# Performance work log

Measured on AMD Instinct MI355X. Metric: run time of the kernel, lower is better.

The kernel has to match this reference:

```python
import jax, jax.numpy as jnp
import numpy as np
import math

IN_SIZE = 4096
OUT_SIZE = 4096
NNZ = 4_194_304
BATCH = 4096


def setup_inputs() -> dict:
    key = jax.random.key(0)
    k_x, k_v, k_i, k_o = jax.random.split(key, 4)
    x = jax.random.normal(k_x, (BATCH, IN_SIZE), dtype=jnp.float32)
    # v = randn(nnz) * (6 / sqrt(in_size + out_size))  (init=None branch)
    scale = 6.0 / math.sqrt(IN_SIZE + OUT_SIZE)
    values = jax.random.normal(k_v, (NNZ,), dtype=jnp.float32) * scale
    idx_in = jax.random.randint(k_i, (NNZ,), 0, IN_SIZE, dtype=jnp.int64 if jax.config.jax_enable_x64 else jnp.int32)
    idx_out = jax.random.randint(k_o, (NNZ,), 0, OUT_SIZE, dtype=jnp.int64 if jax.config.jax_enable_x64 else jnp.int32)
    return {"x": x, "values": values, "idx_in": idx_in, "idx_out": idx_out}


def reference(x, values, idx_in, idx_out):
    # torch.sparse.mm(W, x.T).T with W = coo((idx_out, idx_in), values, (out, in)).
    # Duplicate (row,col) entries in COO sum, which x.at[...].add reproduces.
    # Scattering into a dense [out, in] matrix (64 MB) is the efficient JAX form;
    # it avoids any [nnz, batch] intermediate and then uses one dense GEMM.
    W = jnp.zeros((OUT_SIZE, IN_SIZE), dtype=values.dtype).at[idx_out, idx_in].add(values)
    return x @ W.T  # [batch, out_size]
```

## Files before the change

kernel.cpp:

```cpp
#include <hip/hip_runtime.h>
#include <hip/hip_bf16.h>

#define IN_SIZE 4096
#define OUT_SIZE 4096
#define BATCH 4096

#define NBLK 512
#define CHUNK 8192
#define NCELL 1024
#define CELLCAP 8192

typedef __bf16 bf16x8 __attribute__((ext_vector_type(8)));
typedef float f32x4 __attribute__((ext_vector_type(4)));

__global__ __launch_bounds__(256) void zero_kernel(int* __restrict__ cellcnt) {
    cellcnt[blockIdx.x * 256 + threadIdx.x & 1023] = 0;
}

__global__ __launch_bounds__(512) void scatres_kernel(const float* __restrict__ vals,
                                                      const int* __restrict__ iin,
                                                      const int* __restrict__ iout,
                                                      int* __restrict__ cellcnt,
                                                      uint2* __restrict__ bkt, int nnz) {
    __shared__ int sout[CHUNK];
    __shared__ int hist[NCELL];
    __shared__ int gbase[NCELL];
    const int b = blockIdx.x, tid = threadIdx.x;
    const int base = b * CHUNK;

    for (int c = tid; c < NCELL; c += 512) hist[c] = 0;
    __syncthreads();

    const int4* io4 = (const int4*)(iout + base);
    for (int i = tid; i < CHUNK / 4; i += 512) {
        if (base + i * 4 + 3 < nnz) {
            const int4 o = io4[i];
            ((int4*)sout)[i] = o;
            atomicAdd(&hist[o.x >> 2], 1);
            atomicAdd(&hist[o.y >> 2], 1);
            atomicAdd(&hist[o.z >> 2], 1);
            atomicAdd(&hist[o.w >> 2], 1);
        } else {
            for (int j = 0; j < 4; ++j) {
                const int k = base + i * 4 + j;
                if (k < nnz) {
                    const int o = iout[k];
                    sout[i * 4 + j] = o;
                    atomicAdd(&hist[o >> 2], 1);
                }
            }
        }
    }
    __syncthreads();

    for (int c = tid; c < NCELL; c += 512)
        gbase[c] = hist[c] ? atomicAdd(&cellcnt[c], hist[c]) : 0;
    __syncthreads();

    const float4* v4 = (const float4*)(vals + base);
    const int4*   a4 = (const int4*)(iin + base);
    for (int i = tid; i < CHUNK / 4; i += 512) {
        if (base + i * 4 + 3 < nnz) {
            const float4 v = v4[i];
            const int4   a = a4[i];
            const int4   o = ((const int4*)sout)[i];
            int c, l; uint2 e;
            c = o.x >> 2; l = atomicSub(&hist[c], 1) - 1;
            e.x = __builtin_bit_cast(unsigned, v.x); e.y = (unsigned)(((o.x & 3) << 12) | a.x);
            bkt[(size_t)c * CELLCAP + gbase[c] + l] = e;
            c = o.y >> 2; l = atomicSub(&hist[c], 1) - 1;
            e.x = __builtin_bit_cast(unsigned, v.y); e.y = (unsigned)(((o.y & 3) << 12) | a.y);
            bkt[(size_t)c * CELLCAP + gbase[c] + l] = e;
            c = o.z >> 2; l = atomicSub(&hist[c], 1) - 1;
            e.x = __builtin_bit_cast(unsigned, v.z); e.y = (unsigned)(((o.z & 3) << 12) | a.z);
            bkt[(size_t)c * CELLCAP + gbase[c] + l] = e;
            c = o.w >> 2; l = atomicSub(&hist[c], 1) - 1;
            e.x = __builtin_bit_cast(unsigned, v.w); e.y = (unsigned)(((o.w & 3) << 12) | a.w);
            bkt[(size_t)c * CELLCAP + gbase[c] + l] = e;
        } else {
            for (int j = 0; j < 4; ++j) {
                const int k = base + i * 4 + j;
                if (k < nnz) {
                    const int o = sout[i * 4 + j];
                    const int c = o >> 2;
                    const int l = atomicSub(&hist[c], 1) - 1;
                    uint2 e;
                    e.x = __builtin_bit_cast(unsigned, vals[k]);
                    e.y = (unsigned)(((o & 3) << 12) | iin[k]);
                    bkt[(size_t)c * CELLCAP + gbase[c] + l] = e;
                }
            }
        }
    }
}

__global__ __launch_bounds__(512) void accum_kernel(const uint2* __restrict__ bkt,
                                                    const int* __restrict__ cellcnt,
                                                    __bf16* __restrict__ W,
                                                    const f32x4* __restrict__ xin,
                                                    bf16x8* __restrict__ xout) {
    __shared__ float acc[4 * 4096];
    const int cell = blockIdx.x, tid = threadIdx.x;
    for (int t = tid; t < 4 * 4096; t += 512) acc[t] = 0.f;
    int n = cellcnt[cell];
    if (n > CELLCAP) n = CELLCAP;
    __syncthreads();

    const uint2* seg = bkt + (size_t)cell * CELLCAP;
    for (int s = tid; s < n; s += 512) {
        const uint2 e = seg[s];
        atomicAdd(&acc[((e.y >> 12) & 3u) * 4096 + (e.y & 0xFFFu)],
                  __builtin_bit_cast(float, e.x));
    }
    __syncthreads();

    bf16x8* out = (bf16x8*)(W + (size_t)cell * 4 * 4096);
    for (int t = tid; t < 2048; t += 512) {
        bf16x8 o;
#pragma unroll
        for (int j = 0; j < 8; ++j) o[j] = (__bf16)acc[t * 8 + j];
        out[t] = o;
    }

    const int xbase = blockIdx.x * 2048;
    for (int t = tid; t < 2048; t += 512) {
        const int idx = xbase + t;
        const f32x4 a = xin[2 * idx];
        const f32x4 bq = xin[2 * idx + 1];
        bf16x8 o;
        o[0] = (__bf16)a[0];  o[1] = (__bf16)a[1];  o[2] = (__bf16)a[2];  o[3] = (__bf16)a[3];
        o[4] = (__bf16)bq[0]; o[5] = (__bf16)bq[1]; o[6] = (__bf16)bq[2]; o[7] = (__bf16)bq[3];
        xout[idx] = o;
    }
}


#define GLL(SRC, DST)                                                         \
    __builtin_amdgcn_global_load_lds(                                         \
        (const __attribute__((address_space(1))) void*)(SRC),                 \
        (__attribute__((address_space(3))) void*)(DST), 16, 0, 0)

#define STAGE_AB(T, BUF)                                                      \
  do {                                                                        \
    const __bf16* sa_ = gA0 + (size_t)(T) * 32;                               \
    __bf16* da_ = &smem[(BUF) * 16384 + tid * 8];                             \
    GLL(sa_, da_);                                                            \
    GLL(sa_ + (size_t)524288, da_ + 4096);                                    \
    const __bf16* sb_ = gB0 + (size_t)(T) * 32;                               \
    __bf16* db_ = &smem[(BUF) * 16384 + 8192 + tid * 8];                      \
    GLL(sb_, db_);                                                            \
    GLL(sb_ + (size_t)524288, db_ + 4096);                                    \
  } while (0)

#define VMW4  asm volatile("s_waitcnt vmcnt(4)" ::: "memory")
#define VMW0  asm volatile("s_waitcnt vmcnt(0)" ::: "memory")
#define VMWN  ((void)0)

#define LBFR(D, BUF)                                                          \
    _Pragma("unroll") for (int j_ = 0; j_ < 4; ++j_)                          \
        D[j_] = *(const bf16x8*)(smem + (BUF) * 16384 + offB[j_])
#define LA03(D, BUF)                                                          \
    _Pragma("unroll") for (int i_ = 0; i_ < 4; ++i_)                          \
        D[i_] = *(const bf16x8*)(smem + (BUF) * 16384 + offA[i_])
#define LA47(BUF)                                                             \
    _Pragma("unroll") for (int i_ = 0; i_ < 4; ++i_)                          \
        af47[i_] = *(const bf16x8*)(smem + (BUF) * 16384 + offA[4 + i_])

#define MFMA_C1(CA, CB)                                                       \
    _Pragma("unroll") for (int i_ = 0; i_ < 4; ++i_)                          \
        _Pragma("unroll") for (int j_ = 0; j_ < 4; ++j_)                      \
            acc[i_][j_] = __builtin_amdgcn_mfma_f32_16x16x32_bf16(            \
                CA[i_], CB[j_], acc[i_][j_], 0, 0, 0)
#define MFMA_C2(CB)                                                           \
    _Pragma("unroll") for (int i_ = 0; i_ < 4; ++i_)                          \
        _Pragma("unroll") for (int j_ = 0; j_ < 4; ++j_)                      \
            acc[4 + i_][j_] = __builtin_amdgcn_mfma_f32_16x16x32_bf16(        \
                af47[i_], CB[j_], acc[4 + i_][j_], 0, 0, 0)

#define ITER(T, BUFC, BUFN, CB, CA, NB, NA, DOSTAGE, SBUF, VMW, DOBAR)        \
  do {                                                                        \
    if (DOSTAGE) STAGE_AB((T) + 3, SBUF);                                     \
    LA47(BUFC);                                                               \
    MFMA_C1(CA, CB);                                                          \
    LBFR(NB, BUFN);                                                           \
    LA03(NA, BUFN);                                                           \
    MFMA_C2(CB);                                                              \
    VMW;                                                                      \
    if (DOBAR) __builtin_amdgcn_s_barrier();                                  \
  } while (0)

__global__ __launch_bounds__(512, 2) void gemm_bt_kernel(
    const __bf16* __restrict__ A,
    const __bf16* __restrict__ B,
    float* __restrict__ C) {
    __shared__ __bf16 smem[4 * 16384];

    const int tid   = threadIdx.x;
    const int lane  = tid & 63;
    const int wv    = tid >> 6;
    const int wm    = wv >> 2;
    const int wn    = wv & 3;
    const int row16 = lane & 15;
    const int quad  = lane >> 4;

    const int swz = (blockIdx.x & 7) * 32 + (blockIdx.x >> 3);
    const int bm  = (swz >> 4) * 256;
    const int bn  = (swz & 15) * 256;

    const int sr = tid >> 2;
    const int sq = (tid & 3) ^ ((sr >> 1) & 3);
    const __bf16* gA0 = A + (size_t)(bm + sr) * 4096 + sq * 8;
    const __bf16* gB0 = B + (size_t)(bn + sr) * 4096 + sq * 8;

    int offA[8], offB[4];
#pragma unroll
    for (int i = 0; i < 8; ++i) {
        const int ra = wm * 128 + i * 16 + row16;
        offA[i] = ra * 32 + ((quad ^ ((ra >> 1) & 3)) * 8);
    }
#pragma unroll
    for (int j = 0; j < 4; ++j) {
        const int rb = wn * 64 + j * 16 + row16;
        offB[j] = 8192 + rb * 32 + ((quad ^ ((rb >> 1) & 3)) * 8);
    }

    f32x4  acc[8][4] = {};
    bf16x8 bfr0[4], a0_[4], bfr1[4], a1_[4], af47[4];

    STAGE_AB(0, 0); STAGE_AB(1, 1); STAGE_AB(2, 2);
    VMW4;
    __builtin_amdgcn_s_barrier();
    LBFR(bfr0, 0);
    LA03(a0_, 0);

    for (int c = 0; c < 31; ++c) {
        const int tb = c * 4;
        ITER(tb + 0, 0, 1, bfr0, a0_, bfr1, a1_, 1, 3, VMW4, 1);
        ITER(tb + 1, 1, 2, bfr1, a1_, bfr0, a0_, 1, 0, VMW4, 1);
        ITER(tb + 2, 2, 3, bfr0, a0_, bfr1, a1_, 1, 1, VMW4, 1);
        ITER(tb + 3, 3, 0, bfr1, a1_, bfr0, a0_, 1, 2, VMW4, 1);
    }
    ITER(124, 0, 1, bfr0, a0_, bfr1, a1_, 1, 3, VMW4, 1);
    ITER(125, 1, 2, bfr1, a1_, bfr0, a0_, 0, 0, VMW0, 1);
    ITER(126, 2, 3, bfr0, a0_, bfr1, a1_, 0, 0, VMWN, 0);
    LA47(3);
    MFMA_C1(a1_, bfr1);
    MFMA_C2(bfr1);

#pragma unroll
    for (int i = 0; i < 8; ++i) {
        const int rbase = bm + wm * 128 + i * 16 + quad * 4;
#pragma unroll
        for (int j = 0; j < 4; ++j) {
            const int col = bn + wn * 64 + j * 16 + row16;
#pragma unroll
            for (int r = 0; r < 4; ++r)
                C[(size_t)(rbase + r) * 4096 + col] = acc[i][j][r];
        }
    }
}

extern "C" void kernel_launch(void* const* d_in, const int* in_sizes, int n_in,
                              void* d_out, int out_size, void* d_ws, size_t ws_size,
                              hipStream_t stream) {
    const float* x    = (const float*)d_in[0];
    const float* vals = (const float*)d_in[1];
    const int*   iin  = (const int*)d_in[2];
    const int*   iout = (const int*)d_in[3];
    float*       C    = (float*)d_out;
    const int    nnz  = in_sizes[1];

    char*   ws      = (char*)d_ws;
    __bf16* Wb      = (__bf16*)ws;
    __bf16* Xb      = (__bf16*)(ws + ((size_t)32 << 20));
    int*    cellcnt = (int*)(ws + ((size_t)64 << 20));
    uint2*  bkt     = (uint2*)d_out;

    zero_kernel<<<4, 256, 0, stream>>>(cellcnt);
    scatres_kernel<<<NBLK, 512, 0, stream>>>(vals, iin, iout, cellcnt, bkt, nnz);
    accum_kernel<<<NCELL, 512, 0, stream>>>(bkt, cellcnt, Wb, (const f32x4*)x, (bf16x8*)Xb);
    gemm_bt_kernel<<<256, 512, 0, stream>>>(Xb, Wb, C);
}
```

Measured before the change: 337.2 us.

## Restructure GEMM main loop into barrier-separated phases with MFMA priority boosts

Replaces the register double-buffered fragment pipeline with a phased schedule: each K-step loads A0-3 and B fragments, issues half the global-to-LDS staging, barriers, then runs MFMAs at raised wave priority, and repeats for A4-7 and the other staging half. Splitting the A and B staging across phases and using s_setprio is meant to keep the waves in lockstep and interleave memory with MFMA work across the two resident blocks. This drops the cross-iteration register prefetch and adds several barriers per step, which could expose LDS read latency.

```diff
diff --git a/kernel.cpp b/kernel.cpp
--- a/kernel.cpp
+++ b/kernel.cpp
@@ -140,12 +140,16 @@
         (const __attribute__((address_space(1))) void*)(SRC),                 \
         (__attribute__((address_space(3))) void*)(DST), 16, 0, 0)
 
-#define STAGE_AB(T, BUF)                                                      \
+#define STAGE_A2(T, BUF)                                                      \
   do {                                                                        \
     const __bf16* sa_ = gA0 + (size_t)(T) * 32;                               \
     __bf16* da_ = &smem[(BUF) * 16384 + tid * 8];                             \
     GLL(sa_, da_);                                                            \
     GLL(sa_ + (size_t)524288, da_ + 4096);                                    \
+  } while (0)
+
+#define STAGE_B2(T, BUF)                                                      \
+  do {                                                                        \
     const __bf16* sb_ = gB0 + (size_t)(T) * 32;                               \
     __bf16* db_ = &smem[(BUF) * 16384 + 8192 + tid * 8];                      \
     GLL(sb_, db_);                                                            \
@@ -155,38 +159,47 @@
 #define VMW4  asm volatile("s_waitcnt vmcnt(4)" ::: "memory")
 #define VMW0  asm volatile("s_waitcnt vmcnt(0)" ::: "memory")
 #define VMWN  ((void)0)
-
-#define LBFR(D, BUF)                                                          \
+#define PH_BAR __builtin_amdgcn_s_barrier()
+
+#define LBFR(BUF)                                                             \
     _Pragma("unroll") for (int j_ = 0; j_ < 4; ++j_)                          \
-        D[j_] = *(const bf16x8*)(smem + (BUF) * 16384 + offB[j_])
-#define LA03(D, BUF)                                                          \
-    _Pragma("unroll") for (int i_ = 0; i_ < 4; ++i_)                          \
-        D[i_] = *(const bf16x8*)(smem + (BUF) * 16384 + offA[i_])
+        bfr[j_] = *(const bf16x8*)(smem + (BUF) * 16384 + offB[j_])
+#define LA03(BUF)                                                             \
+    _Pragma("unroll") for (int i_ = 0; i_ < 4; ++i_)                          \
+        af03[i_] = *(const bf16x8*)(smem + (BUF) * 16384 + offA[i_])
 #define LA47(BUF)                                                             \
     _Pragma("unroll") for (int i_ = 0; i_ < 4; ++i_)                          \
         af47[i_] = *(const bf16x8*)(smem + (BUF) * 16384 + offA[4 + i_])
 
-#define MFMA_C1(CA, CB)                                                       \
+#define MFMA_C1                                                               \
     _Pragma("unroll") for (int i_ = 0; i_ < 4; ++i_)                          \
         _Pragma("unroll") for (int j_ = 0; j_ < 4; ++j_)                      \
             acc[i_][j_] = __builtin_amdgcn_mfma_f32_16x16x32_bf16(            \
-                CA[i_], CB[j_], acc[i_][j_], 0, 0, 0)
-#define MFMA_C2(CB)                                                           \
+                af03[i_], bfr[j_], acc[i_][j_], 0, 0, 0)
+#define MFMA_C2                                                               \
     _Pragma("unroll") for (int i_ = 0; i_ < 4; ++i_)                          \
         _Pragma("unroll") for (int j_ = 0; j_ < 4; ++j_)                      \
             acc[4 + i_][j_] = __builtin_amdgcn_mfma_f32_16x16x32_bf16(        \
-                af47[i_], CB[j_], acc[4 + i_][j_], 0, 0, 0)
-
-#define ITER(T, BUFC, BUFN, CB, CA, NB, NA, DOSTAGE, SBUF, VMW, DOBAR)        \
+                af47[i_], bfr[j_], acc[4 + i_][j_], 0, 0, 0)
+
+#define ITER(T, BUF, SBUF, DOSTAGE, VMW, ENDBAR)                              \
   do {                                                                        \
-    if (DOSTAGE) STAGE_AB((T) + 3, SBUF);                                     \
-    LA47(BUFC);                                                               \
-    MFMA_C1(CA, CB);                                                          \
-    LBFR(NB, BUFN);                                                           \
-    LA03(NA, BUFN);                                                           \
-    MFMA_C2(CB);                                                              \
+    LBFR(BUF);                                                                \
+    LA03(BUF);                                                                \
+    if (DOSTAGE) STAGE_A2((T) + 3, SBUF);                                     \
+    PH_BAR;                                                                   \
+    __builtin_amdgcn_s_setprio(1);                                            \
+    MFMA_C1;                                                                  \
+    __builtin_amdgcn_s_setprio(0);                                            \
+    PH_BAR;                                                                   \
+    LA47(BUF);                                                                \
+    if (DOSTAGE) STAGE_B2((T) + 3, SBUF);                                     \
+    PH_BAR;                                                                   \
+    __builtin_amdgcn_s_setprio(1);                                            \
+    MFMA_C2;                                                                  \
+    __builtin_amdgcn_s_setprio(0);                                            \
     VMW;                                                                      \
-    if (DOBAR) __builtin_amdgcn_s_barrier();                                  \
+    if (ENDBAR) PH_BAR;                                                       \
   } while (0)
 
 __global__ __launch_bounds__(512, 2) void gemm_bt_kernel(
@@ -225,27 +238,25 @@
     }
 
     f32x4  acc[8][4] = {};
-    bf16x8 bfr0[4], a0_[4], bfr1[4], a1_[4], af47[4];
-
-    STAGE_AB(0, 0); STAGE_AB(1, 1); STAGE_AB(2, 2);
+    bf16x8 bfr[4], af03[4], af47[4];
+
+    STAGE_A2(0, 0); STAGE_B2(0, 0);
+    STAGE_A2(1, 1); STAGE_B2(1, 1);
+    STAGE_A2(2, 2); STAGE_B2(2, 2);
     VMW4;
-    __builtin_amdgcn_s_barrier();
-    LBFR(bfr0, 0);
-    LA03(a0_, 0);
+    PH_BAR;
 
     for (int c = 0; c < 31; ++c) {
         const int tb = c * 4;
-        ITER(tb + 0, 0, 1, bfr0, a0_, bfr1, a1_, 1, 3, VMW4, 1);
-        ITER(tb + 1, 1, 2, bfr1, a1_, bfr0, a0_, 1, 0, VMW4, 1);
-        ITER(tb + 2, 2, 3, bfr0, a0_, bfr1, a1_, 1, 1, VMW4, 1);
-        ITER(tb + 3, 3, 0, bfr1, a1_, bfr0, a0_, 1, 2, VMW4, 1);
-    }
-    ITER(124, 0, 1, bfr0, a0_, bfr1, a1_, 1, 3, VMW4, 1);
-    ITER(125, 1, 2, bfr1, a1_, bfr0, a0_, 0, 0, VMW0, 1);
-    ITER(126, 2, 3, bfr0, a0_, bfr1, a1_, 0, 0, VMWN, 0);
-    LA47(3);
-    MFMA_C1(a1_, bfr1);
-    MFMA_C2(bfr1);
+        ITER(tb + 0, 0, 3, 1, VMW4, 1);
+        ITER(tb + 1, 1, 0, 1, VMW4, 1);
+        ITER(tb + 2, 2, 1, 1, VMW4, 1);
+        ITER(tb + 3, 3, 2, 1, VMW4, 1);
+    }
+    ITER(124, 0, 3, 1, VMW4, 1);
+    ITER(125, 1, 0, 0, VMW4, 1);
+    ITER(126, 2, 0, 0, VMW0, 1);
+    ITER(127, 3, 0, 0, VMWN, 0);
 
 #pragma unroll
     for (int i = 0; i < 8; ++i) {
```

New measurement: 343.1 us. Within noise of the previous version (+1.8%).

## Switch GEMM inner loop from 16x16x32 to 32x32x16 bf16 MFMA tiles

Applied to the files above, without the earlier changes.

Replaces the 16x16x32 MFMA decomposition of each wave's 128x64 sub-tile with 32x32x16 MFMAs. Each K=32 step is split into two K=16 halves, and the LDS fragment loads are restructured into two phases with new swizzled offsets. Fewer, larger MFMAs need fewer LDS fragment reads per FLOP, which is meant to cut LDS traffic and instruction-issue overhead. The epilogue is rewritten to match the 32x32 accumulator layout; this adds register-layout complexity and could change bank-conflict behavior.

```diff
diff --git a/kernel.cpp b/kernel.cpp
--- a/kernel.cpp
+++ b/kernel.cpp
@@ -12,6 +12,7 @@
 
 typedef __bf16 bf16x8 __attribute__((ext_vector_type(8)));
 typedef float f32x4 __attribute__((ext_vector_type(4)));
+typedef float f32x16 __attribute__((ext_vector_type(16)));
 
 __global__ __launch_bounds__(256) void zero_kernel(int* __restrict__ cellcnt) {
     cellcnt[blockIdx.x * 256 + threadIdx.x & 1023] = 0;
@@ -156,35 +157,39 @@
 #define VMW0  asm volatile("s_waitcnt vmcnt(0)" ::: "memory")
 #define VMWN  ((void)0)
 
-#define LBFR(D, BUF)                                                          \
-    _Pragma("unroll") for (int j_ = 0; j_ < 4; ++j_)                          \
-        D[j_] = *(const bf16x8*)(smem + (BUF) * 16384 + offB[j_])
-#define LA03(D, BUF)                                                          \
-    _Pragma("unroll") for (int i_ = 0; i_ < 4; ++i_)                          \
-        D[i_] = *(const bf16x8*)(smem + (BUF) * 16384 + offA[i_])
-#define LA47(BUF)                                                             \
-    _Pragma("unroll") for (int i_ = 0; i_ < 4; ++i_)                          \
-        af47[i_] = *(const bf16x8*)(smem + (BUF) * 16384 + offA[4 + i_])
-
-#define MFMA_C1(CA, CB)                                                       \
-    _Pragma("unroll") for (int i_ = 0; i_ < 4; ++i_)                          \
-        _Pragma("unroll") for (int j_ = 0; j_ < 4; ++j_)                      \
-            acc[i_][j_] = __builtin_amdgcn_mfma_f32_16x16x32_bf16(            \
-                CA[i_], CB[j_], acc[i_][j_], 0, 0, 0)
-#define MFMA_C2(CB)                                                           \
-    _Pragma("unroll") for (int i_ = 0; i_ < 4; ++i_)                          \
-        _Pragma("unroll") for (int j_ = 0; j_ < 4; ++j_)                      \
-            acc[4 + i_][j_] = __builtin_amdgcn_mfma_f32_16x16x32_bf16(        \
-                af47[i_], CB[j_], acc[4 + i_][j_], 0, 0, 0)
-
-#define ITER(T, BUFC, BUFN, CB, CA, NB, NA, DOSTAGE, SBUF, VMW, DOBAR)        \
+#define LS0(AD, BD, BUF)                                                      \
+  do {                                                                        \
+    _Pragma("unroll") for (int i_ = 0; i_ < 4; ++i_)                          \
+        AD[i_] = *(const bf16x8*)(smem + (BUF) * 16384 + offA0[i_]);          \
+    _Pragma("unroll") for (int j_ = 0; j_ < 2; ++j_)                          \
+        BD[j_] = *(const bf16x8*)(smem + (BUF) * 16384 + offB0[j_]);          \
+  } while (0)
+#define LS1(BUF)                                                              \
+  do {                                                                        \
+    _Pragma("unroll") for (int i_ = 0; i_ < 4; ++i_)                          \
+        a1s[i_] = *(const bf16x8*)(smem + (BUF) * 16384 + offA1[i_]);         \
+    _Pragma("unroll") for (int j_ = 0; j_ < 2; ++j_)                          \
+        b1s[j_] = *(const bf16x8*)(smem + (BUF) * 16384 + offB1[j_]);         \
+  } while (0)
+
+#define MFMA_S0(AD, BD)                                                       \
+    _Pragma("unroll") for (int i_ = 0; i_ < 4; ++i_)                          \
+        _Pragma("unroll") for (int j_ = 0; j_ < 2; ++j_)                      \
+            acc[i_][j_] = __builtin_amdgcn_mfma_f32_32x32x16_bf16(            \
+                AD[i_], BD[j_], acc[i_][j_], 0, 0, 0)
+#define MFMA_S1                                                               \
+    _Pragma("unroll") for (int i_ = 0; i_ < 4; ++i_)                          \
+        _Pragma("unroll") for (int j_ = 0; j_ < 2; ++j_)                      \
+            acc[i_][j_] = __builtin_amdgcn_mfma_f32_32x32x16_bf16(            \
+                a1s[i_], b1s[j_], acc[i_][j_], 0, 0, 0)
+
+#define ITER(T, BUFC, BUFN, B0C, A0C, B0N, A0N, DOSTAGE, SBUF, VMW, DOBAR)    \
   do {                                                                        \
     if (DOSTAGE) STAGE_AB((T) + 3, SBUF);                                     \
-    LA47(BUFC);                                                               \
-    MFMA_C1(CA, CB);                                                          \
-    LBFR(NB, BUFN);                                                           \
-    LA03(NA, BUFN);                                                           \
-    MFMA_C2(CB);                                                              \
+    LS1(BUFC);                                                                \
+    MFMA_S0(A0C, B0C);                                                        \
+    LS0(A0N, B0N, BUFN);                                                      \
+    MFMA_S1;                                                                  \
     VMW;                                                                      \
     if (DOBAR) __builtin_amdgcn_s_barrier();                                  \
   } while (0)
@@ -200,8 +205,8 @@
     const int wv    = tid >> 6;
     const int wm    = wv >> 2;
     const int wn    = wv & 3;
-    const int row16 = lane & 15;
-    const int quad  = lane >> 4;
+    const int col32 = lane & 31;
+    const int half  = lane >> 5;
 
     const int swz = (blockIdx.x & 7) * 32 + (blockIdx.x >> 3);
     const int bm  = (swz >> 4) * 256;
@@ -212,50 +217,53 @@
     const __bf16* gA0 = A + (size_t)(bm + sr) * 4096 + sq * 8;
     const __bf16* gB0 = B + (size_t)(bn + sr) * 4096 + sq * 8;
 
-    int offA[8], offB[4];
-#pragma unroll
-    for (int i = 0; i < 8; ++i) {
-        const int ra = wm * 128 + i * 16 + row16;
-        offA[i] = ra * 32 + ((quad ^ ((ra >> 1) & 3)) * 8);
-    }
-#pragma unroll
-    for (int j = 0; j < 4; ++j) {
-        const int rb = wn * 64 + j * 16 + row16;
-        offB[j] = 8192 + rb * 32 + ((quad ^ ((rb >> 1) & 3)) * 8);
-    }
-
-    f32x4  acc[8][4] = {};
-    bf16x8 bfr0[4], a0_[4], bfr1[4], a1_[4], af47[4];
+    int offA0[4], offA1[4], offB0[2], offB1[2];
+#pragma unroll
+    for (int i = 0; i < 4; ++i) {
+        const int ra = wm * 128 + i * 32 + col32;
+        offA0[i] = ra * 32 + (((0 + half) ^ ((ra >> 1) & 3)) * 8);
+        offA1[i] = ra * 32 + (((2 + half) ^ ((ra >> 1) & 3)) * 8);
+    }
+#pragma unroll
+    for (int j = 0; j < 2; ++j) {
+        const int rb = wn * 64 + j * 32 + col32;
+        offB0[j] = 8192 + rb * 32 + (((0 + half) ^ ((rb >> 1) & 3)) * 8);
+        offB1[j] = 8192 + rb * 32 + (((2 + half) ^ ((rb >> 1) & 3)) * 8);
+    }
+
+    f32x16 acc[4][2] = {};
+    bf16x8 a0_[4], b0_[2], a1_[4], b1_[2], a1s[4], b1s[2];
 
     STAGE_AB(0, 0); STAGE_AB(1, 1); STAGE_AB(2, 2);
     VMW4;
     __builtin_amdgcn_s_barrier();
-    LBFR(bfr0, 0);
-    LA03(a0_, 0);
+    LS0(a0_, b0_, 0);
 
     for (int c = 0; c < 31; ++c) {
         const int tb = c * 4;
-        ITER(tb + 0, 0, 1, bfr0, a0_, bfr1, a1_, 1, 3, VMW4, 1);
-        ITER(tb + 1, 1, 2, bfr1, a1_, bfr0, a0_, 1, 0, VMW4, 1);
-        ITER(tb + 2, 2, 3, bfr0, a0_, bfr1, a1_, 1, 1, VMW4, 1);
-        ITER(tb + 3, 3, 0, bfr1, a1_, bfr0, a0_, 1, 2, VMW4, 1);
-    }
-    ITER(124, 0, 1, bfr0, a0_, bfr1, a1_, 1, 3, VMW4, 1);
-    ITER(125, 1, 2, bfr1, a1_, bfr0, a0_, 0, 0, VMW0, 1);
-    ITER(126, 2, 3, bfr0, a0_, bfr1, a1_, 0, 0, VMWN, 0);
-    LA47(3);
-    MFMA_C1(a1_, bfr1);
-    MFMA_C2(bfr1);
-
-#pragma unroll
-    for (int i = 0; i < 8; ++i) {
-        const int rbase = bm + wm * 128 + i * 16 + quad * 4;
-#pragma unroll
-        for (int j = 0; j < 4; ++j) {
-            const int col = bn + wn * 64 + j * 16 + row16;
-#pragma unroll
-            for (int r = 0; r < 4; ++r)
-                C[(size_t)(rbase + r) * 4096 + col] = acc[i][j][r];
+        ITER(tb + 0, 0, 1, b0_, a0_, b1_, a1_, 1, 3, VMW4, 1);
+        ITER(tb + 1, 1, 2, b1_, a1_, b0_, a0_, 1, 0, VMW4, 1);
+        ITER(tb + 2, 2, 3, b0_, a0_, b1_, a1_, 1, 1, VMW4, 1);
+        ITER(tb + 3, 3, 0, b1_, a1_, b0_, a0_, 1, 2, VMW4, 1);
+    }
+    ITER(124, 0, 1, b0_, a0_, b1_, a1_, 1, 3, VMW4, 1);
+    ITER(125, 1, 2, b1_, a1_, b0_, a0_, 0, 0, VMW0, 1);
+    ITER(126, 2, 3, b0_, a0_, b1_, a1_, 0, 0, VMWN, 0);
+    LS1(3);
+    MFMA_S0(a1_, b1_);
+    MFMA_S1;
+
+#pragma unroll
+    for (int i = 0; i < 4; ++i) {
+#pragma unroll
+        for (int j = 0; j < 2; ++j) {
+            const int colg = bn + wn * 64 + j * 32 + col32;
+#pragma unroll
+            for (int r = 0; r < 16; ++r) {
+                const int rowg = bm + wm * 128 + i * 32 +
+                                 (r & 3) + 8 * (r >> 2) + 4 * half;
+                C[(size_t)rowg * 4096 + colg] = acc[i][j][r];
+            }
         }
     }
 }
```

New measurement: 348.9 us. 1.03x slower.
